# Kernel optimization log

Measured on AMD Instinct MI355X. Metric: run time of the kernel, lower is better.

The kernel has to match this reference:

```python
import jax, jax.numpy as jnp
import numpy as np

B, N, F_IN, DIM, TOPK = 64, 1024, 10, 64, 20
EPS = 1e-5  # BatchNorm eps
NEG_SLOPE = 0.2


def _bn_eval(x, gamma, beta, mean, var):
    # eval-mode BatchNorm1d over the channel (last) axis
    return (x - mean) * jax.lax.rsqrt(var + EPS) * gamma + beta


def setup_inputs() -> dict:
    key = jax.random.key(0)
    ks = jax.random.split(key, 10)
    return {
        "data": jax.random.normal(ks[0], (B, N, F_IN), jnp.float32),
        "emb": jax.random.normal(ks[1], (N, DIM), jnp.float32),
        "W_lin": jax.random.normal(ks[2], (F_IN, DIM), jnp.float32),
        "att_i": jax.random.normal(ks[3], (DIM,), jnp.float32),
        "att_j": jax.random.normal(ks[4], (DIM,), jnp.float32),
        "att_em_i": jax.random.normal(ks[5], (DIM,), jnp.float32),
        "att_em_j": jax.random.normal(ks[6], (DIM,), jnp.float32),
        "gnn_bias": jax.random.normal(ks[7], (DIM,), jnp.float32),
        "bn1_gamma": jnp.ones((DIM,), jnp.float32),
        "bn1_beta": jnp.zeros((DIM,), jnp.float32),
        "bn1_mean": jnp.zeros((DIM,), jnp.float32),
        "bn1_var": jnp.ones((DIM,), jnp.float32),
        "bn2_gamma": jnp.ones((DIM,), jnp.float32),
        "bn2_beta": jnp.zeros((DIM,), jnp.float32),
        "bn2_mean": jnp.zeros((DIM,), jnp.float32),
        "bn2_var": jnp.ones((DIM,), jnp.float32),
        "out_W": jax.random.normal(ks[8], (DIM, 1), jnp.float32),
        "out_b": jax.random.normal(ks[9], (1,), jnp.float32),
    }


def reference(data, emb, W_lin, att_i, att_j, att_em_i, att_em_j, gnn_bias,
              bn1_gamma, bn1_beta, bn1_mean, bn1_var,
              bn2_gamma, bn2_beta, bn2_mean, bn2_var, out_W, out_b):
    Bn, Nn, _ = data.shape
    BN_nodes = Bn * Nn
    x = data.reshape(BN_nodes, -1)                      # [B*N, F_IN] (input is detached in torch)

    # ---- dynamic graph: cosine similarity of (detached) node embeddings, top-k per row ----
    w = jax.lax.stop_gradient(emb)                      # weights_arr = embedding.detach()
    norms = jnp.linalg.norm(w, axis=-1)                 # [N]
    cos = (w @ w.T) / (norms[:, None] * norms[None, :])  # [N, N]
    topk_idx = jax.lax.top_k(cos, TOPK)[1]              # [N, K], gated_j (message sources)
    src = topk_idx.reshape(-1)                          # j
    dst = jnp.repeat(jnp.arange(Nn), TOPK)              # i
    offs = (jnp.arange(Bn) * Nn)[:, None]               # per-graph node offsets
    bsrc = (src[None, :] + offs).reshape(-1)            # [B*N*K]
    bdst = (dst[None, :] + offs).reshape(-1)
    self_mask = bsrc == bdst                            # edges killed by remove_self_loops
    loops = jnp.arange(BN_nodes)                        # add_self_loops
    e_src = jnp.concatenate([bsrc, loops])              # [E]
    e_dst = jnp.concatenate([bdst, loops])
    e_mask = jnp.concatenate([self_mask, jnp.zeros(BN_nodes, bool)])

    # ---- GAT-style attention message passing (heads=1, concat=False, aggr='add') ----
    h = x @ W_lin                                       # [B*N, DIM]
    h_i, h_j = h[e_dst], h[e_src]                       # gathers, [E, DIM]
    emb_i = emb[e_dst % Nn]                             # embedding repeated per batch graph
    emb_j = emb[e_src % Nn]
    logit = (h_i * att_i).sum(-1) + (emb_i * att_em_i).sum(-1) \
          + (h_j * att_j).sum(-1) + (emb_j * att_em_j).sum(-1)  # [E]
    logit = jnp.where(logit > 0, logit, NEG_SLOPE * logit)       # leaky_relu(0.2)
    logit = jnp.where(e_mask, -1e30, logit)             # removed self-loops get zero weight
    seg_max = jax.ops.segment_max(logit, e_dst, num_segments=BN_nodes)
    ex = jnp.where(e_mask, 0.0, jnp.exp(logit - seg_max[e_dst]))
    seg_sum = jax.ops.segment_sum(ex, e_dst, num_segments=BN_nodes)
    alpha = ex / seg_sum[e_dst]                         # segment softmax over incoming edges
    agg = jax.ops.segment_sum(h_j * alpha[:, None], e_dst, num_segments=BN_nodes)
    agg = agg + gnn_bias                                # [B*N, DIM]
    gcn = jax.nn.relu(_bn_eval(agg, bn1_gamma, bn1_beta, bn1_mean, bn1_var))

    # ---- output head: multiply by node embedding, BN+ReLU, Linear(DIM->1) ----
    y = gcn.reshape(Bn, Nn, DIM) * emb[None, :, :]
    y = jax.nn.relu(_bn_eval(y, bn2_gamma, bn2_beta, bn2_mean, bn2_var))
    out = y @ out_W + out_b                             # [B, N, 1]; dropout is inference no-op
    return out.reshape(Bn, Nn)
```

## Files before the change

### kernel.cpp

```cpp
#include <hip/hip_runtime.h>

#define N_NODES 1024
#define B_SZ 64
#define F_IN 10
#define DIM 64
#define TOPK 20
#define BN_TOT (B_SZ * N_NODES)

__global__ __launch_bounds__(256) void k_gemm_g(const float* __restrict__ emb,
                                               float* __restrict__ g) {
    __shared__ float As[64][65];
    __shared__ float Bs[64][65];
    const int r0 = blockIdx.y * 64, c0 = blockIdx.x * 64;
    const int t = threadIdx.x;
#pragma unroll
    for (int k = 0; k < 16; ++k) {
        int idx = t + k * 256;
        int rr = idx >> 6, cc = idx & 63;
        As[rr][cc] = emb[(r0 + rr) * DIM + cc];
        Bs[rr][cc] = emb[(c0 + rr) * DIM + cc];
    }
    __syncthreads();
    const int tx = t & 15, ty = t >> 4;
    float acc[4][4] = {};
#pragma unroll 8
    for (int d = 0; d < 64; ++d) {
        float a[4], b[4];
#pragma unroll
        for (int ii = 0; ii < 4; ++ii) a[ii] = As[ty * 4 + ii][d];
#pragma unroll
        for (int jj = 0; jj < 4; ++jj) b[jj] = Bs[tx * 4 + jj][d];
#pragma unroll
        for (int ii = 0; ii < 4; ++ii)
#pragma unroll
            for (int jj = 0; jj < 4; ++jj) acc[ii][jj] += a[ii] * b[jj];
    }
#pragma unroll
    for (int ii = 0; ii < 4; ++ii)
#pragma unroll
        for (int jj = 0; jj < 4; ++jj)
            g[(r0 + ty * 4 + ii) * N_NODES + (c0 + tx * 4 + jj)] = acc[ii][jj];
}

__global__ __launch_bounds__(256) void k_prep(
    const float* __restrict__ emb,
    const float* __restrict__ att_em_i, const float* __restrict__ att_em_j,
    const float* __restrict__ gnn_bias,
    const float* __restrict__ g1, const float* __restrict__ b1,
    const float* __restrict__ m1, const float* __restrict__ v1,
    const float* __restrict__ g2, const float* __restrict__ b2,
    const float* __restrict__ m2, const float* __restrict__ v2,
    float* __restrict__ edi, float* __restrict__ esi, float* __restrict__ nrm,
    float4* __restrict__ bnp) {
    const int node = blockIdx.x * 4 + (threadIdx.x >> 6);
    const int d = threadIdx.x & 63;
    float e = emb[node * DIM + d];
    float t1 = e * att_em_i[d];
    float t2 = e * att_em_j[d];
    float t3 = e * e;
#pragma unroll
    for (int m = 32; m >= 1; m >>= 1) {
        t1 += __shfl_xor(t1, m, 64);
        t2 += __shfl_xor(t2, m, 64);
        t3 += __shfl_xor(t3, m, 64);
    }
    if (d == 0) { edi[node] = t1; esi[node] = t2; nrm[node] = sqrtf(t3); }
    if (blockIdx.x == 0 && threadIdx.x < DIM) {
        const int q = threadIdx.x;
        float a1 = g1[q] * rsqrtf(v1[q] + 1e-5f);
        float c1 = (gnn_bias[q] - m1[q]) * a1 + b1[q];
        float a2 = g2[q] * rsqrtf(v2[q] + 1e-5f);
        float c2 = b2[q] - m2[q] * a2;
        bnp[q] = make_float4(a1, c1, a2, c2);
    }
}

__global__ __launch_bounds__(256) void k_hscal(
    const float* __restrict__ data, const float* __restrict__ W_lin,
    const float* __restrict__ att_i, const float* __restrict__ att_j,
    const float* __restrict__ edi, const float* __restrict__ esi,
    float* __restrict__ h, float* __restrict__ dd, float* __restrict__ ss) {
    const int node = blockIdx.x * 4 + (threadIdx.x >> 6);
    const int d = threadIdx.x & 63;
    const int i = node & (N_NODES - 1);
    float hv = 0.f;
#pragma unroll
    for (int f = 0; f < F_IN; ++f)
        hv = fmaf(data[node * F_IN + f], W_lin[f * DIM + d], hv);
    h[node * DIM + d] = hv;
    float s1 = hv * att_i[d];
    float s2 = hv * att_j[d];
#pragma unroll
    for (int m = 32; m >= 1; m >>= 1) {
        s1 += __shfl_xor(s1, m, 64);
        s2 += __shfl_xor(s2, m, 64);
    }
    if (d == 0) { dd[node] = s1 + edi[i]; ss[node] = s2 + esi[i]; }
}

__global__ __launch_bounds__(256) void k_topk(const float* __restrict__ g,
                                              const float* __restrict__ nrm,
                                              int* __restrict__ tk) {
    __shared__ float lv[4];
    __shared__ int li[4];
    const int i = blockIdx.x;
    const int t = threadIdx.x;
    const int lane = t & 63, w = t >> 6;
    const float ni = nrm[i];
    float4 gv = ((const float4*)(g + (size_t)i * N_NODES))[t];
    float4 nv = ((const float4*)nrm)[t];
    float v[4];
    v[0] = gv.x / (ni * nv.x);
    v[1] = gv.y / (ni * nv.y);
    v[2] = gv.z / (ni * nv.z);
    v[3] = gv.w / (ni * nv.w);
    for (int it = 0; it < TOPK; ++it) {
        float bv = v[0];
        int bq = 0;
#pragma unroll
        for (int q = 1; q < 4; ++q)
            if (v[q] > bv) { bv = v[q]; bq = q; }
        int bidx = t * 4 + bq;
#pragma unroll
        for (int m = 32; m >= 1; m >>= 1) {
            float ov = __shfl_xor(bv, m, 64);
            int oi = __shfl_xor(bidx, m, 64);
            if (ov > bv || (ov == bv && oi < bidx)) { bv = ov; bidx = oi; }
        }
        if (lane == 0) { lv[w] = bv; li[w] = bidx; }
        __syncthreads();
        float wv = lv[0];
        int wi = li[0];
#pragma unroll
        for (int q = 1; q < 4; ++q)
            if (lv[q] > wv || (lv[q] == wv && li[q] < wi)) { wv = lv[q]; wi = li[q]; }
        if (t == (wi >> 2)) v[wi & 3] = -3.0e38f;
        if (t == 0) tk[i * TOPK + it] = wi;
        __syncthreads();
    }
}

__global__ __launch_bounds__(256) void k_main(
    const float* __restrict__ h, const float* __restrict__ emb,
    const float* __restrict__ dd, const float* __restrict__ ss,
    const int* __restrict__ tk, const float4* __restrict__ bnp,
    const float* __restrict__ outW, const float* __restrict__ outB,
    float* __restrict__ out) {
    __shared__ int jbuf[4][24];
    __shared__ float abuf[4][24];
    const int bid = blockIdx.x;
    const int nb = (bid & 7) * 2048 + (bid >> 3);
    const int w = threadIdx.x >> 6, lane = threadIdx.x & 63;
    const int node = nb * 4 + w;
    const int i = node & (N_NODES - 1);
    const int bbase = node & ~(N_NODES - 1);

    int j = i;
    if (lane < TOPK) j = tk[i * TOPK + lane];
    if (lane <= TOPK) jbuf[w][lane] = j;
    __builtin_amdgcn_wave_barrier();
    int4 jj4[5];
#pragma unroll
    for (int q = 0; q < 5; ++q) jj4[q] = ((int4*)jbuf[w])[q];
    int j20 = jbuf[w][20];

    const float* hb = h + (size_t)bbase * DIM + lane;
    float hv[21];
#pragma unroll
    for (int q = 0; q < 5; ++q) {
        hv[4 * q + 0] = hb[jj4[q].x * DIM];
        hv[4 * q + 1] = hb[jj4[q].y * DIM];
        hv[4 * q + 2] = hb[jj4[q].z * DIM];
        hv[4 * q + 3] = hb[jj4[q].w * DIM];
    }
    hv[20] = hb[j20 * DIM];

    const bool masked = (lane < TOPK) && (j == i);
    float lg = -3.0e38f;
    if (lane <= TOPK) {
        float l = dd[node] + ss[bbase + j];
        l = (l > 0.f) ? l : 0.2f * l;
        lg = masked ? -3.0e38f : l;
    }
    float m = lg;
#pragma unroll
    for (int mm = 16; mm >= 1; mm >>= 1) m = fmaxf(m, __shfl_xor(m, mm, 64));
    float ex = (lane <= TOPK && !masked) ? __expf(lg - m) : 0.f;
    float s = ex;
#pragma unroll
    for (int mm = 16; mm >= 1; mm >>= 1) s += __shfl_xor(s, mm, 64);
    const float alpha = ex / s;
    if (lane <= TOPK) abuf[w][lane] = alpha;
    __builtin_amdgcn_wave_barrier();
    float4 aa4[5];
#pragma unroll
    for (int q = 0; q < 5; ++q) aa4[q] = ((float4*)abuf[w])[q];
    float a20 = abuf[w][20];

    float agg = 0.f;
#pragma unroll
    for (int q = 0; q < 5; ++q) {
        agg = fmaf(aa4[q].x, hv[4 * q + 0], agg);
        agg = fmaf(aa4[q].y, hv[4 * q + 1], agg);
        agg = fmaf(aa4[q].z, hv[4 * q + 2], agg);
        agg = fmaf(aa4[q].w, hv[4 * q + 3], agg);
    }
    agg = fmaf(a20, hv[20], agg);

    const float4 p = bnp[lane];
    float x1 = fmaxf(fmaf(agg, p.x, p.y), 0.f);
    float y = x1 * emb[i * DIM + lane];
    float x2 = fmaxf(fmaf(y, p.z, p.w), 0.f);
    float o = x2 * outW[lane];
#pragma unroll
    for (int mm = 32; mm >= 1; mm >>= 1) o += __shfl_xor(o, mm, 64);
    if (lane == 0) out[node] = o + outB[0];
}

extern "C" void kernel_launch(void* const* d_in, const int* in_sizes, int n_in,
                              void* d_out, int out_size, void* d_ws, size_t ws_size,
                              hipStream_t stream) {
    const float* data     = (const float*)d_in[0];
    const float* emb      = (const float*)d_in[1];
    const float* W_lin    = (const float*)d_in[2];
    const float* att_i    = (const float*)d_in[3];
    const float* att_j    = (const float*)d_in[4];
    const float* att_em_i = (const float*)d_in[5];
    const float* att_em_j = (const float*)d_in[6];
    const float* gnn_bias = (const float*)d_in[7];
    const float* g1 = (const float*)d_in[8];
    const float* b1 = (const float*)d_in[9];
    const float* m1 = (const float*)d_in[10];
    const float* v1 = (const float*)d_in[11];
    const float* g2 = (const float*)d_in[12];
    const float* b2 = (const float*)d_in[13];
    const float* m2 = (const float*)d_in[14];
    const float* v2 = (const float*)d_in[15];
    const float* outW = (const float*)d_in[16];
    const float* outB = (const float*)d_in[17];
    float* out = (float*)d_out;

    float* ws = (float*)d_ws;
    float* g     = ws;
    float* h     = ws + (1 << 20);
    float* dd    = h + (size_t)BN_TOT * DIM;
    float* ss    = dd + BN_TOT;
    float* edi   = ss + BN_TOT;
    float* esi   = edi + N_NODES;
    float* nrm   = esi + N_NODES;
    int*   tk    = (int*)(nrm + N_NODES);
    float4* bnp  = (float4*)(tk + N_NODES * TOPK);

    k_gemm_g<<<dim3(16, 16), 256, 0, stream>>>(emb, g);
    k_prep<<<N_NODES / 4, 256, 0, stream>>>(emb, att_em_i, att_em_j, gnn_bias,
                                            g1, b1, m1, v1, g2, b2, m2, v2,
                                            edi, esi, nrm, bnp);
    k_hscal<<<BN_TOT / 4, 256, 0, stream>>>(data, W_lin, att_i, att_j, edi, esi,
                                            h, dd, ss);
    k_topk<<<N_NODES, 256, 0, stream>>>(g, nrm, tk);
    k_main<<<BN_TOT / 4, 256, 0, stream>>>(h, emb, dd, ss, tk, bnp, outW, outB, out);
}
```

Before: 82.47 us.

## Fuse gemm, prep and hscal into one launch; two-level top-k selection

Merges the cosine-Gram GEMM, the per-node embedding scalars and the h/attention-scalar kernels into a single heterogeneous launch, with block ranges selecting the role. The embedding attention terms move into k_main so hscal no longer depends on prep. hscal now handles 4 nodes per wave and loads W_lin into registers once. Top-k changes from 20 block-wide barrier rounds to per-wave local top-20 followed by a single-wave merge, removing 40 __syncthreads per row at the cost of extra per-wave selection work.

```diff
diff --git a/kernel.cpp b/kernel.cpp
--- a/kernel.cpp
+++ b/kernel.cpp
@@ -7,102 +7,116 @@
 #define TOPK 20
 #define BN_TOT (B_SZ * N_NODES)
 
-__global__ __launch_bounds__(256) void k_gemm_g(const float* __restrict__ emb,
-                                               float* __restrict__ g) {
-    __shared__ float As[64][65];
-    __shared__ float Bs[64][65];
-    const int r0 = blockIdx.y * 64, c0 = blockIdx.x * 64;
-    const int t = threadIdx.x;
-#pragma unroll
-    for (int k = 0; k < 16; ++k) {
-        int idx = t + k * 256;
-        int rr = idx >> 6, cc = idx & 63;
-        As[rr][cc] = emb[(r0 + rr) * DIM + cc];
-        Bs[rr][cc] = emb[(c0 + rr) * DIM + cc];
-    }
-    __syncthreads();
-    const int tx = t & 15, ty = t >> 4;
-    float acc[4][4] = {};
-#pragma unroll 8
-    for (int d = 0; d < 64; ++d) {
-        float a[4], b[4];
-#pragma unroll
-        for (int ii = 0; ii < 4; ++ii) a[ii] = As[ty * 4 + ii][d];
-#pragma unroll
-        for (int jj = 0; jj < 4; ++jj) b[jj] = Bs[tx * 4 + jj][d];
-#pragma unroll
-        for (int ii = 0; ii < 4; ++ii)
-#pragma unroll
-            for (int jj = 0; jj < 4; ++jj) acc[ii][jj] += a[ii] * b[jj];
-    }
-#pragma unroll
-    for (int ii = 0; ii < 4; ++ii)
-#pragma unroll
-        for (int jj = 0; jj < 4; ++jj)
-            g[(r0 + ty * 4 + ii) * N_NODES + (c0 + tx * 4 + jj)] = acc[ii][jj];
-}
-
-__global__ __launch_bounds__(256) void k_prep(
-    const float* __restrict__ emb,
+#define GEMM_BLKS 256
+#define PREP_BLKS 256
+#define HSCAL_BLKS 4096
+
+__global__ __launch_bounds__(256) void k_build(
+    const float* __restrict__ data, const float* __restrict__ emb,
+    const float* __restrict__ W_lin,
+    const float* __restrict__ att_i, const float* __restrict__ att_j,
     const float* __restrict__ att_em_i, const float* __restrict__ att_em_j,
     const float* __restrict__ gnn_bias,
     const float* __restrict__ g1, const float* __restrict__ b1,
     const float* __restrict__ m1, const float* __restrict__ v1,
     const float* __restrict__ g2, const float* __restrict__ b2,
     const float* __restrict__ m2, const float* __restrict__ v2,
+    float* __restrict__ g, float* __restrict__ h,
+    float* __restrict__ dd, float* __restrict__ ss,
     float* __restrict__ edi, float* __restrict__ esi, float* __restrict__ nrm,
     float4* __restrict__ bnp) {
-    const int node = blockIdx.x * 4 + (threadIdx.x >> 6);
-    const int d = threadIdx.x & 63;
-    float e = emb[node * DIM + d];
-    float t1 = e * att_em_i[d];
-    float t2 = e * att_em_j[d];
-    float t3 = e * e;
-#pragma unroll
-    for (int m = 32; m >= 1; m >>= 1) {
-        t1 += __shfl_xor(t1, m, 64);
-        t2 += __shfl_xor(t2, m, 64);
-        t3 += __shfl_xor(t3, m, 64);
-    }
-    if (d == 0) { edi[node] = t1; esi[node] = t2; nrm[node] = sqrtf(t3); }
-    if (blockIdx.x == 0 && threadIdx.x < DIM) {
-        const int q = threadIdx.x;
-        float a1 = g1[q] * rsqrtf(v1[q] + 1e-5f);
-        float c1 = (gnn_bias[q] - m1[q]) * a1 + b1[q];
-        float a2 = g2[q] * rsqrtf(v2[q] + 1e-5f);
-        float c2 = b2[q] - m2[q] * a2;
-        bnp[q] = make_float4(a1, c1, a2, c2);
-    }
-}
-
-__global__ __launch_bounds__(256) void k_hscal(
-    const float* __restrict__ data, const float* __restrict__ W_lin,
-    const float* __restrict__ att_i, const float* __restrict__ att_j,
-    const float* __restrict__ edi, const float* __restrict__ esi,
-    float* __restrict__ h, float* __restrict__ dd, float* __restrict__ ss) {
-    const int node = blockIdx.x * 4 + (threadIdx.x >> 6);
-    const int d = threadIdx.x & 63;
-    const int i = node & (N_NODES - 1);
-    float hv = 0.f;
-#pragma unroll
-    for (int f = 0; f < F_IN; ++f)
-        hv = fmaf(data[node * F_IN + f], W_lin[f * DIM + d], hv);
-    h[node * DIM + d] = hv;
-    float s1 = hv * att_i[d];
-    float s2 = hv * att_j[d];
-#pragma unroll
-    for (int m = 32; m >= 1; m >>= 1) {
-        s1 += __shfl_xor(s1, m, 64);
-        s2 += __shfl_xor(s2, m, 64);
-    }
-    if (d == 0) { dd[node] = s1 + edi[i]; ss[node] = s2 + esi[i]; }
+    const int bid = blockIdx.x;
+    const int t = threadIdx.x;
+    const int lane = t & 63, w = t >> 6;
+
+    if (bid < GEMM_BLKS) {
+        __shared__ float As[64][65];
+        __shared__ float Bs[64][65];
+        const int r0 = (bid >> 4) * 64, c0 = (bid & 15) * 64;
+#pragma unroll
+        for (int k = 0; k < 16; ++k) {
+            int idx = t + k * 256;
+            int rr = idx >> 6, cc = idx & 63;
+            As[rr][cc] = emb[(r0 + rr) * DIM + cc];
+            Bs[rr][cc] = emb[(c0 + rr) * DIM + cc];
+        }
+        __syncthreads();
+        const int tx = t & 15, ty = t >> 4;
+        float acc[4][4] = {};
+#pragma unroll 8
+        for (int d = 0; d < 64; ++d) {
+            float a[4], b[4];
+#pragma unroll
+            for (int ii = 0; ii < 4; ++ii) a[ii] = As[ty * 4 + ii][d];
+#pragma unroll
+            for (int jj = 0; jj < 4; ++jj) b[jj] = Bs[tx * 4 + jj][d];
+#pragma unroll
+            for (int ii = 0; ii < 4; ++ii)
+#pragma unroll
+                for (int jj = 0; jj < 4; ++jj) acc[ii][jj] += a[ii] * b[jj];
+        }
+#pragma unroll
+        for (int ii = 0; ii < 4; ++ii)
+#pragma unroll
+            for (int jj = 0; jj < 4; ++jj)
+                g[(r0 + ty * 4 + ii) * N_NODES + (c0 + tx * 4 + jj)] = acc[ii][jj];
+        return;
+    }
+
+    if (bid < GEMM_BLKS + PREP_BLKS) {
+        const int node = (bid - GEMM_BLKS) * 4 + w;
+        float e = emb[node * DIM + lane];
+        float t1 = e * att_em_i[lane];
+        float t2 = e * att_em_j[lane];
+        float t3 = e * e;
+#pragma unroll
+        for (int m = 32; m >= 1; m >>= 1) {
+            t1 += __shfl_xor(t1, m, 64);
+            t2 += __shfl_xor(t2, m, 64);
+            t3 += __shfl_xor(t3, m, 64);
+        }
+        if (lane == 0) { edi[node] = t1; esi[node] = t2; nrm[node] = sqrtf(t3); }
+        if (bid == GEMM_BLKS && t < DIM) {
+            float a1 = g1[t] * rsqrtf(v1[t] + 1e-5f);
+            float c1 = (gnn_bias[t] - m1[t]) * a1 + b1[t];
+            float a2 = g2[t] * rsqrtf(v2[t] + 1e-5f);
+            float c2 = b2[t] - m2[t] * a2;
+            bnp[t] = make_float4(a1, c1, a2, c2);
+        }
+        return;
+    }
+
+    {
+        const int base = (bid - GEMM_BLKS - PREP_BLKS) * 16 + w * 4;
+        float wl[F_IN];
+#pragma unroll
+        for (int f = 0; f < F_IN; ++f) wl[f] = W_lin[f * DIM + lane];
+        const float ai = att_i[lane], aj = att_j[lane];
+#pragma unroll
+        for (int r = 0; r < 4; ++r) {
+            const int node = base + r;
+            const float* dp = data + node * F_IN;
+            float hv = 0.f;
+#pragma unroll
+            for (int f = 0; f < F_IN; ++f) hv = fmaf(dp[f], wl[f], hv);
+            h[node * DIM + lane] = hv;
+            float s1 = hv * ai;
+            float s2 = hv * aj;
+#pragma unroll
+            for (int m = 32; m >= 1; m >>= 1) {
+                s1 += __shfl_xor(s1, m, 64);
+                s2 += __shfl_xor(s2, m, 64);
+            }
+            if (lane == 0) { dd[node] = s1; ss[node] = s2; }
+        }
+    }
 }
 
 __global__ __launch_bounds__(256) void k_topk(const float* __restrict__ g,
                                               const float* __restrict__ nrm,
                                               int* __restrict__ tk) {
-    __shared__ float lv[4];
-    __shared__ int li[4];
+    __shared__ float cv[4][20];
+    __shared__ int ci[4][20];
     const int i = blockIdx.x;
     const int t = threadIdx.x;
     const int lane = t & 63, w = t >> 6;
@@ -127,22 +141,43 @@
             int oi = __shfl_xor(bidx, m, 64);
             if (ov > bv || (ov == bv && oi < bidx)) { bv = ov; bidx = oi; }
         }
-        if (lane == 0) { lv[w] = bv; li[w] = bidx; }
-        __syncthreads();
-        float wv = lv[0];
-        int wi = li[0];
-#pragma unroll
-        for (int q = 1; q < 4; ++q)
-            if (lv[q] > wv || (lv[q] == wv && li[q] < wi)) { wv = lv[q]; wi = li[q]; }
-        if (t == (wi >> 2)) v[wi & 3] = -3.0e38f;
-        if (t == 0) tk[i * TOPK + it] = wi;
-        __syncthreads();
+        if (lane == 0) { cv[w][it] = bv; ci[w][it] = bidx; }
+        if ((bidx >> 2) == t) v[bidx & 3] = -3.0e38f;
+    }
+    __syncthreads();
+    if (w == 0) {
+        float mv[4];
+        int mi[4];
+#pragma unroll
+        for (int q = 0; q < 4; ++q) {
+            if (lane < TOPK) { mv[q] = cv[q][lane]; mi[q] = ci[q][lane]; }
+            else { mv[q] = -3.0e38f; mi[q] = 0x7fffffff; }
+        }
+        for (int it = 0; it < TOPK; ++it) {
+            float bv = mv[0];
+            int bq = 0;
+#pragma unroll
+            for (int q = 1; q < 4; ++q)
+                if (mv[q] > bv || (mv[q] == bv && mi[q] < mi[bq])) { bv = mv[q]; bq = q; }
+            int bidx = mi[bq];
+#pragma unroll
+            for (int m = 32; m >= 1; m >>= 1) {
+                float ov = __shfl_xor(bv, m, 64);
+                int oi = __shfl_xor(bidx, m, 64);
+                if (ov > bv || (ov == bv && oi < bidx)) { bv = ov; bidx = oi; }
+            }
+            if (lane == 0) tk[i * TOPK + it] = bidx;
+#pragma unroll
+            for (int q = 0; q < 4; ++q)
+                if (mi[q] == bidx) mv[q] = -3.0e38f;
+        }
     }
 }
 
 __global__ __launch_bounds__(256) void k_main(
     const float* __restrict__ h, const float* __restrict__ emb,
     const float* __restrict__ dd, const float* __restrict__ ss,
+    const float* __restrict__ edi, const float* __restrict__ esi,
     const int* __restrict__ tk, const float4* __restrict__ bnp,
     const float* __restrict__ outW, const float* __restrict__ outB,
     float* __restrict__ out) {
@@ -176,9 +211,10 @@
     hv[20] = hb[j20 * DIM];
 
     const bool masked = (lane < TOPK) && (j == i);
+    const float dde = dd[node] + edi[i];
     float lg = -3.0e38f;
     if (lane <= TOPK) {
-        float l = dd[node] + ss[bbase + j];
+        float l = dde + ss[bbase + j] + esi[j];
         l = (l > 0.f) ? l : 0.2f * l;
         lg = masked ? -3.0e38f : l;
     }
@@ -251,12 +287,11 @@
     int*   tk    = (int*)(nrm + N_NODES);
     float4* bnp  = (float4*)(tk + N_NODES * TOPK);
 
-    k_gemm_g<<<dim3(16, 16), 256, 0, stream>>>(emb, g);
-    k_prep<<<N_NODES / 4, 256, 0, stream>>>(emb, att_em_i, att_em_j, gnn_bias,
-                                            g1, b1, m1, v1, g2, b2, m2, v2,
-                                            edi, esi, nrm, bnp);
-    k_hscal<<<BN_TOT / 4, 256, 0, stream>>>(data, W_lin, att_i, att_j, edi, esi,
-                                            h, dd, ss);
+    k_build<<<GEMM_BLKS + PREP_BLKS + HSCAL_BLKS, 256, 0, stream>>>(
+        data, emb, W_lin, att_i, att_j, att_em_i, att_em_j, gnn_bias,
+        g1, b1, m1, v1, g2, b2, m2, v2,
+        g, h, dd, ss, edi, esi, nrm, bnp);
     k_topk<<<N_NODES, 256, 0, stream>>>(g, nrm, tk);
-    k_main<<<BN_TOT / 4, 256, 0, stream>>>(h, emb, dd, ss, tk, bnp, outW, outB, out);
-}
+    k_main<<<BN_TOT / 4, 256, 0, stream>>>(h, emb, dd, ss, edi, esi, tk, bnp,
+                                           outW, outB, out);
+}
```

Result: no change. 83.98 us (+1.8%).
